# Performance work log

Hardware: AMD Instinct MI355X
Metric: run time of the kernel (lower is better)

## Reference

```python
import jax, jax.numpy as jnp
import numpy as np
import math

B, L = 32, 4096
INPUT_SIZE, QUERY_SIZE, VALUE_SIZE, H = 1024, 64, 256, 16
DV = INPUT_SIZE // H  # per-head value dim = 64


def setup_inputs() -> dict:
    key = jax.random.key(0)
    ks = jax.random.split(key, 7)
    s_q = 1.0 / math.sqrt(INPUT_SIZE)
    s_v = 1.0 / math.sqrt(VALUE_SIZE)
    return {
        "query": jax.random.normal(ks[0], (B, INPUT_SIZE), jnp.float32),
        "key": jax.random.normal(ks[1], (B, L, QUERY_SIZE), jnp.float32),
        "value": jax.random.normal(ks[2], (B, L, VALUE_SIZE), jnp.float32),
        # query_heads: Linear(input_size, head_num*query_size) with bias
        "Wq": jax.random.uniform(ks[3], (H * QUERY_SIZE, INPUT_SIZE), jnp.float32, -s_q, s_q),
        "bq": jax.random.uniform(ks[4], (H * QUERY_SIZE,), jnp.float32, -s_q, s_q),
        # value_proj: Linear(value_size, input_size) with bias (concatenate=True)
        "Wv": jax.random.uniform(ks[5], (INPUT_SIZE, VALUE_SIZE), jnp.float32, -s_v, s_v),
        "bv": jax.random.uniform(ks[6], (INPUT_SIZE,), jnp.float32, -s_v, s_v),
    }


def reference(query, key, value, Wq, bq, Wv, bv):
    # value projection: (B, L, input_size) -> (B, H, L, DV)
    v = jnp.einsum("bld,ed->ble", value, Wv) + bv
    v = v.reshape(B, L, H, DV).transpose(0, 2, 1, 3)
    # query projection: (B, input_size) -> (B, H, QUERY_SIZE)
    q = (query @ Wq.T + bq).reshape(B, H, QUERY_SIZE)
    # scores: (B, H, L); key shared across heads
    scores = jnp.einsum("bhd,bld->bhl", q, key) / math.sqrt(QUERY_SIZE)
    p = jax.nn.softmax(scores, axis=-1)
    # weighted sum: (B, H, DV) -> concat -> (B, input_size)
    out = jnp.einsum("bhl,bhld->bhd", p, v)
    return out.reshape(B, H * DV)
```

## Files before the change

### kernel.cpp

```cpp
#include <hip/hip_runtime.h>
#include <math.h>

#define B_   32
#define L_   4096
#define IN_  1024
#define QS_  64
#define VS_  256
#define H_   16

#define Q_OFF 0
#define M_OFF 32768

__device__ __forceinline__ float dot4(float4 a, float4 b) {
    return a.x*b.x + a.y*b.y + a.z*b.z + a.w*b.w;
}

__global__ __launch_bounds__(256) void qproj_kernel(
        const float* __restrict__ query, const float* __restrict__ Wq,
        const float* __restrict__ bq, float* __restrict__ ws) {
    const int t = threadIdx.x;
    const int g = blockIdx.x * 256 + t;
    const int o = g >> 2, sub = g & 3;
    const int b = o >> 10, c = o & 1023;

    const float4* wq4 = (const float4*)(Wq + (size_t)c * IN_) + sub * 64;
    const float4* q4  = (const float4*)(query + (size_t)b * IN_) + sub * 64;
    float4 acc = make_float4(0.f, 0.f, 0.f, 0.f);
    #pragma unroll 8
    for (int k = 0; k < 64; ++k) {
        float4 w = wq4[k], q = q4[k];
        acc.x += w.x * q.x; acc.y += w.y * q.y;
        acc.z += w.z * q.z; acc.w += w.w * q.w;
    }
    float r = acc.x + acc.y + acc.z + acc.w;
    r += __shfl_xor(r, 1);
    r += __shfl_xor(r, 2);
    if (sub == 0) ws[Q_OFF + b * 1024 + c] = (r + bq[c]) * 0.125f;
}

template<int CL>
__global__ __launch_bounds__(256, 4) void attn_chunk_kernel(
        const float* __restrict__ key, const float* __restrict__ value,
        float* __restrict__ ws) {
    constexpr int NCH = L_ / CL;
    constexpr int R   = CL / 64;
    constexpr int S_OFF   = M_OFF + B_ * NCH * H_;
    constexpr int CTX_OFF = S_OFF + B_ * NCH * H_;

    __shared__ float4 qs4[256];
    __shared__ float4 ps4[4 * CL];

    const int t  = threadIdx.x;
    const int ch = blockIdx.x, b = blockIdx.y;
    const int lm = t & 63, w = t >> 6;
    const int l0 = ch * CL;

    qs4[t] = ((const float4*)(ws + Q_OFF + (size_t)b * IN_))[t];
    __syncthreads();

    const float* keyb = key + ((size_t)b * L_ + l0) * QS_;
    float s[R][4];
    #pragma unroll
    for (int j = 0; j < R; ++j)
        #pragma unroll
        for (int hh = 0; hh < 4; ++hh) s[j][hh] = 0.f;

    #pragma unroll
    for (int e4 = 0; e4 < 16; ++e4) {
        float4 qv[4];
        #pragma unroll
        for (int hh = 0; hh < 4; ++hh) qv[hh] = qs4[(4 * w + hh) * 16 + e4];
        #pragma unroll
        for (int j = 0; j < R; ++j) {
            float4 kv = *(const float4*)(keyb + (size_t)(R * lm + j) * QS_ + e4 * 4);
            #pragma unroll
            for (int hh = 0; hh < 4; ++hh) s[j][hh] += dot4(kv, qv[hh]);
        }
    }

    float m[4];
    #pragma unroll
    for (int hh = 0; hh < 4; ++hh) {
        float v = s[0][hh];
        #pragma unroll
        for (int j = 1; j < R; ++j) v = fmaxf(v, s[j][hh]);
        #pragma unroll
        for (int off = 32; off >= 1; off >>= 1) v = fmaxf(v, __shfl_xor(v, off));
        m[hh] = v;
    }

    float p[R][4];
    #pragma unroll
    for (int j = 0; j < R; ++j)
        #pragma unroll
        for (int hh = 0; hh < 4; ++hh) p[j][hh] = __expf(s[j][hh] - m[hh]);

    float sum[4];
    #pragma unroll
    for (int hh = 0; hh < 4; ++hh) {
        float v = p[0][hh];
        #pragma unroll
        for (int j = 1; j < R; ++j) v += p[j][hh];
        #pragma unroll
        for (int off = 32; off >= 1; off >>= 1) v += __shfl_xor(v, off);
        sum[hh] = v;
    }
    if (lm == 0) {
        #pragma unroll
        for (int hh = 0; hh < 4; ++hh) {
            ws[M_OFF + (b * NCH + ch) * H_ + 4 * w + hh] = m[hh];
            ws[S_OFF + (b * NCH + ch) * H_ + 4 * w + hh] = sum[hh];
        }
    }

    #pragma unroll
    for (int j = 0; j < R; ++j)
        ps4[w * CL + R * lm + j] = make_float4(p[j][0], p[j][1], p[j][2], p[j][3]);

    float4 ctx[4];
    #pragma unroll
    for (int hh = 0; hh < 4; ++hh) ctx[hh] = make_float4(0.f, 0.f, 0.f, 0.f);

    const float*  valb = value + ((size_t)b * L_ + l0) * VS_;
    const float4* psw  = ps4 + w * CL;
    for (int i0 = 0; i0 < CL; i0 += 8) {
        float4 vv[8], pv[8];
        #pragma unroll
        for (int u = 0; u < 8; ++u)
            vv[u] = *(const float4*)(valb + (size_t)(i0 + u) * VS_ + 4 * lm);
        #pragma unroll
        for (int u = 0; u < 8; ++u) pv[u] = psw[i0 + u];
        #pragma unroll
        for (int u = 0; u < 8; ++u) {
            const float* ph = (const float*)&pv[u];
            #pragma unroll
            for (int hh = 0; hh < 4; ++hh) {
                ctx[hh].x += ph[hh] * vv[u].x;
                ctx[hh].y += ph[hh] * vv[u].y;
                ctx[hh].z += ph[hh] * vv[u].z;
                ctx[hh].w += ph[hh] * vv[u].w;
            }
        }
    }

    float* ctxw = ws + CTX_OFF + (size_t)((b * NCH + ch) * H_) * VS_;
    #pragma unroll
    for (int hh = 0; hh < 4; ++hh)
        *(float4*)(ctxw + (size_t)(4 * w + hh) * VS_ + 4 * lm) = ctx[hh];
}

template<int CL>
__global__ __launch_bounds__(256) void reduce_proj_kernel(
        const float* __restrict__ Wv, const float* __restrict__ bv,
        const float* __restrict__ ws, float* __restrict__ out) {
    constexpr int NCH = L_ / CL;
    constexpr int S_OFF   = M_OFF + B_ * NCH * H_;
    constexpr int CTX_OFF = S_OFF + B_ * NCH * H_;

    __shared__ __align__(16) float ctx_lds[VS_];
    const int t = threadIdx.x;
    const int b = blockIdx.x >> 4, h = blockIdx.x & 15;

    float M = -1e30f;
    #pragma unroll
    for (int c = 0; c < NCH; ++c)
        M = fmaxf(M, ws[M_OFF + (b * NCH + c) * H_ + h]);

    float S = 0.f, acc = 0.f;
    #pragma unroll 4
    for (int c = 0; c < NCH; ++c) {
        float wgt = __expf(ws[M_OFF + (b * NCH + c) * H_ + h] - M);
        S += ws[S_OFF + (b * NCH + c) * H_ + h] * wgt;
        acc += wgt * ws[CTX_OFF + ((size_t)(b * NCH + c) * H_ + h) * VS_ + t];
    }
    ctx_lds[t] = acc / S;
    __syncthreads();

    const int d = t >> 2, qq = t & 3;
    const float4* wv4 = (const float4*)(Wv + (size_t)(h * 64 + d) * VS_);
    const float4* cl4 = (const float4*)ctx_lds;
    float a = 0.f;
    #pragma unroll
    for (int i = 0; i < 16; ++i) a += dot4(wv4[qq * 16 + i], cl4[qq * 16 + i]);
    a += __shfl_xor(a, 1);
    a += __shfl_xor(a, 2);
    if (qq == 0) out[b * 1024 + h * 64 + d] = a + bv[h * 64 + d];
}

extern "C" void kernel_launch(void* const* d_in, const int* in_sizes, int n_in,
                              void* d_out, int out_size, void* d_ws, size_t ws_size,
                              hipStream_t stream) {
    (void)in_sizes; (void)n_in; (void)out_size;
    const float* query = (const float*)d_in[0];
    const float* key   = (const float*)d_in[1];
    const float* value = (const float*)d_in[2];
    const float* Wq    = (const float*)d_in[3];
    const float* bq    = (const float*)d_in[4];
    const float* Wv    = (const float*)d_in[5];
    const float* bv    = (const float*)d_in[6];
    float* out = (float*)d_out;
    float* ws  = (float*)d_ws;

    qproj_kernel<<<512, 256, 0, stream>>>(query, Wq, bq, ws);

    const size_t need128 = (size_t)(32768 + 2 * B_ * 32 * H_ + (size_t)B_ * 32 * H_ * VS_) * 4;
    if (ws_size >= need128) {
        attn_chunk_kernel<128><<<dim3(32, B_), 256, 0, stream>>>(key, value, ws);
        reduce_proj_kernel<128><<<B_ * H_, 256, 0, stream>>>(Wv, bv, ws, out);
    } else {
        attn_chunk_kernel<256><<<dim3(16, B_), 256, 0, stream>>>(key, value, ws);
        reduce_proj_kernel<256><<<B_ * H_, 256, 0, stream>>>(Wv, bv, ws, out);
    }
}
```

Before: 289.2 us.

## Widen attention blocks to 512 threads and split qproj dot products finer

The attention chunk kernel now uses 512 threads (8 waves), each wave handling 2 heads instead of 4. This halves per-thread score and context accumulators and doubles the waves available to hide value-load latency, at the cost of each wave re-reading the full value chunk (value traffic through cache doubles). The query projection splits each dot product across 16 lanes instead of 4 to spread work over 2048 blocks. The workspace-size fallback path for chunk 256 is removed, so the code assumes the workspace is large enough.

```diff
diff --git a/kernel.cpp b/kernel.cpp
--- a/kernel.cpp
+++ b/kernel.cpp
@@ -7,9 +7,13 @@
 #define QS_  64
 #define VS_  256
 #define H_   16
+#define CL_  128
+#define NCH_ 32
 
-#define Q_OFF 0
-#define M_OFF 32768
+#define Q_OFF   0
+#define M_OFF   32768
+#define S_OFF   (M_OFF + B_ * NCH_ * H_)
+#define CTX_OFF (S_OFF + B_ * NCH_ * H_)
 
 __device__ __forceinline__ float dot4(float4 a, float4 b) {
     return a.x*b.x + a.y*b.y + a.z*b.z + a.w*b.w;
@@ -20,14 +24,14 @@
         const float* __restrict__ bq, float* __restrict__ ws) {
     const int t = threadIdx.x;
     const int g = blockIdx.x * 256 + t;
-    const int o = g >> 2, sub = g & 3;
+    const int o = g >> 4, sub = g & 15;
     const int b = o >> 10, c = o & 1023;
 
-    const float4* wq4 = (const float4*)(Wq + (size_t)c * IN_) + sub * 64;
-    const float4* q4  = (const float4*)(query + (size_t)b * IN_) + sub * 64;
+    const float4* wq4 = (const float4*)(Wq + (size_t)c * IN_) + sub * 16;
+    const float4* q4  = (const float4*)(query + (size_t)b * IN_) + sub * 16;
     float4 acc = make_float4(0.f, 0.f, 0.f, 0.f);
-    #pragma unroll 8
-    for (int k = 0; k < 64; ++k) {
+    #pragma unroll
+    for (int k = 0; k < 16; ++k) {
         float4 w = wq4[k], q = q4[k];
         acc.x += w.x * q.x; acc.y += w.y * q.y;
         acc.z += w.z * q.z; acc.w += w.w * q.w;
@@ -35,143 +39,113 @@
     float r = acc.x + acc.y + acc.z + acc.w;
     r += __shfl_xor(r, 1);
     r += __shfl_xor(r, 2);
+    r += __shfl_xor(r, 4);
+    r += __shfl_xor(r, 8);
     if (sub == 0) ws[Q_OFF + b * 1024 + c] = (r + bq[c]) * 0.125f;
 }
 
-template<int CL>
-__global__ __launch_bounds__(256, 4) void attn_chunk_kernel(
+__global__ __launch_bounds__(512, 8) void attn_chunk_kernel(
         const float* __restrict__ key, const float* __restrict__ value,
         float* __restrict__ ws) {
-    constexpr int NCH = L_ / CL;
-    constexpr int R   = CL / 64;
-    constexpr int S_OFF   = M_OFF + B_ * NCH * H_;
-    constexpr int CTX_OFF = S_OFF + B_ * NCH * H_;
-
     __shared__ float4 qs4[256];
-    __shared__ float4 ps4[4 * CL];
+    __shared__ float2 ps2[8 * CL_];
 
     const int t  = threadIdx.x;
     const int ch = blockIdx.x, b = blockIdx.y;
     const int lm = t & 63, w = t >> 6;
-    const int l0 = ch * CL;
+    const int l0 = ch * CL_;
 
-    qs4[t] = ((const float4*)(ws + Q_OFF + (size_t)b * IN_))[t];
+    if (t < 256) qs4[t] = ((const float4*)(ws + Q_OFF + (size_t)b * IN_))[t];
     __syncthreads();
 
     const float* keyb = key + ((size_t)b * L_ + l0) * QS_;
-    float s[R][4];
-    #pragma unroll
-    for (int j = 0; j < R; ++j)
-        #pragma unroll
-        for (int hh = 0; hh < 4; ++hh) s[j][hh] = 0.f;
-
+    float s[2][2] = {{0.f, 0.f}, {0.f, 0.f}};
     #pragma unroll
     for (int e4 = 0; e4 < 16; ++e4) {
-        float4 qv[4];
+        float4 q0 = qs4[(2 * w) * 16 + e4];
+        float4 q1 = qs4[(2 * w + 1) * 16 + e4];
         #pragma unroll
-        for (int hh = 0; hh < 4; ++hh) qv[hh] = qs4[(4 * w + hh) * 16 + e4];
-        #pragma unroll
-        for (int j = 0; j < R; ++j) {
-            float4 kv = *(const float4*)(keyb + (size_t)(R * lm + j) * QS_ + e4 * 4);
-            #pragma unroll
-            for (int hh = 0; hh < 4; ++hh) s[j][hh] += dot4(kv, qv[hh]);
+        for (int j = 0; j < 2; ++j) {
+            float4 kv = *(const float4*)(keyb + (size_t)(2 * lm + j) * QS_ + e4 * 4);
+            s[j][0] += dot4(kv, q0);
+            s[j][1] += dot4(kv, q1);
         }
     }
 
-    float m[4];
+    float m[2], sum[2], p[2][2];
     #pragma unroll
-    for (int hh = 0; hh < 4; ++hh) {
-        float v = s[0][hh];
-        #pragma unroll
-        for (int j = 1; j < R; ++j) v = fmaxf(v, s[j][hh]);
+    for (int hh = 0; hh < 2; ++hh) {
+        float v = fmaxf(s[0][hh], s[1][hh]);
         #pragma unroll
         for (int off = 32; off >= 1; off >>= 1) v = fmaxf(v, __shfl_xor(v, off));
         m[hh] = v;
     }
-
-    float p[R][4];
     #pragma unroll
-    for (int j = 0; j < R; ++j)
+    for (int j = 0; j < 2; ++j)
         #pragma unroll
-        for (int hh = 0; hh < 4; ++hh) p[j][hh] = __expf(s[j][hh] - m[hh]);
-
-    float sum[4];
+        for (int hh = 0; hh < 2; ++hh) p[j][hh] = __expf(s[j][hh] - m[hh]);
     #pragma unroll
-    for (int hh = 0; hh < 4; ++hh) {
-        float v = p[0][hh];
-        #pragma unroll
-        for (int j = 1; j < R; ++j) v += p[j][hh];
+    for (int hh = 0; hh < 2; ++hh) {
+        float v = p[0][hh] + p[1][hh];
         #pragma unroll
         for (int off = 32; off >= 1; off >>= 1) v += __shfl_xor(v, off);
         sum[hh] = v;
     }
     if (lm == 0) {
         #pragma unroll
-        for (int hh = 0; hh < 4; ++hh) {
-            ws[M_OFF + (b * NCH + ch) * H_ + 4 * w + hh] = m[hh];
-            ws[S_OFF + (b * NCH + ch) * H_ + 4 * w + hh] = sum[hh];
+        for (int hh = 0; hh < 2; ++hh) {
+            ws[M_OFF + (b * NCH_ + ch) * H_ + 2 * w + hh] = m[hh];
+            ws[S_OFF + (b * NCH_ + ch) * H_ + 2 * w + hh] = sum[hh];
         }
     }
 
     #pragma unroll
-    for (int j = 0; j < R; ++j)
-        ps4[w * CL + R * lm + j] = make_float4(p[j][0], p[j][1], p[j][2], p[j][3]);
+    for (int j = 0; j < 2; ++j)
+        ps2[w * CL_ + 2 * lm + j] = make_float2(p[j][0], p[j][1]);
 
-    float4 ctx[4];
-    #pragma unroll
-    for (int hh = 0; hh < 4; ++hh) ctx[hh] = make_float4(0.f, 0.f, 0.f, 0.f);
-
+    float4 ctx0 = make_float4(0.f, 0.f, 0.f, 0.f);
+    float4 ctx1 = make_float4(0.f, 0.f, 0.f, 0.f);
     const float*  valb = value + ((size_t)b * L_ + l0) * VS_;
-    const float4* psw  = ps4 + w * CL;
-    for (int i0 = 0; i0 < CL; i0 += 8) {
-        float4 vv[8], pv[8];
+    const float2* psw  = ps2 + w * CL_;
+    for (int i0 = 0; i0 < CL_; i0 += 4) {
+        float4 vv[4]; float2 pv[4];
         #pragma unroll
-        for (int u = 0; u < 8; ++u)
+        for (int u = 0; u < 4; ++u)
             vv[u] = *(const float4*)(valb + (size_t)(i0 + u) * VS_ + 4 * lm);
         #pragma unroll
-        for (int u = 0; u < 8; ++u) pv[u] = psw[i0 + u];
+        for (int u = 0; u < 4; ++u) pv[u] = psw[i0 + u];
         #pragma unroll
-        for (int u = 0; u < 8; ++u) {
-            const float* ph = (const float*)&pv[u];
-            #pragma unroll
-            for (int hh = 0; hh < 4; ++hh) {
-                ctx[hh].x += ph[hh] * vv[u].x;
-                ctx[hh].y += ph[hh] * vv[u].y;
-                ctx[hh].z += ph[hh] * vv[u].z;
-                ctx[hh].w += ph[hh] * vv[u].w;
-            }
+        for (int u = 0; u < 4; ++u) {
+            ctx0.x += pv[u].x * vv[u].x; ctx0.y += pv[u].x * vv[u].y;
+            ctx0.z += pv[u].x * vv[u].z; ctx0.w += pv[u].x * vv[u].w;
+            ctx1.x += pv[u].y * vv[u].x; ctx1.y += pv[u].y * vv[u].y;
+            ctx1.z += pv[u].y * vv[u].z; ctx1.w += pv[u].y * vv[u].w;
         }
     }
 
-    float* ctxw = ws + CTX_OFF + (size_t)((b * NCH + ch) * H_) * VS_;
-    #pragma unroll
-    for (int hh = 0; hh < 4; ++hh)
-        *(float4*)(ctxw + (size_t)(4 * w + hh) * VS_ + 4 * lm) = ctx[hh];
+    float* ctxw = ws + CTX_OFF + (size_t)((b * NCH_ + ch) * H_) * VS_;
+    *(float4*)(ctxw + (size_t)(2 * w) * VS_ + 4 * lm)     = ctx0;
+    *(float4*)(ctxw + (size_t)(2 * w + 1) * VS_ + 4 * lm) = ctx1;
 }
 
-template<int CL>
 __global__ __launch_bounds__(256) void reduce_proj_kernel(
         const float* __restrict__ Wv, const float* __restrict__ bv,
         const float* __restrict__ ws, float* __restrict__ out) {
-    constexpr int NCH = L_ / CL;
-    constexpr int S_OFF   = M_OFF + B_ * NCH * H_;
-    constexpr int CTX_OFF = S_OFF + B_ * NCH * H_;
-
     __shared__ __align__(16) float ctx_lds[VS_];
     const int t = threadIdx.x;
     const int b = blockIdx.x >> 4, h = blockIdx.x & 15;
 
     float M = -1e30f;
     #pragma unroll
-    for (int c = 0; c < NCH; ++c)
-        M = fmaxf(M, ws[M_OFF + (b * NCH + c) * H_ + h]);
+    for (int c = 0; c < NCH_; ++c)
+        M = fmaxf(M, ws[M_OFF + (b * NCH_ + c) * H_ + h]);
 
     float S = 0.f, acc = 0.f;
     #pragma unroll 4
-    for (int c = 0; c < NCH; ++c) {
-        float wgt = __expf(ws[M_OFF + (b * NCH + c) * H_ + h] - M);
-        S += ws[S_OFF + (b * NCH + c) * H_ + h] * wgt;
-        acc += wgt * ws[CTX_OFF + ((size_t)(b * NCH + c) * H_ + h) * VS_ + t];
+    for (int c = 0; c < NCH_; ++c) {
+        float wgt = __expf(ws[M_OFF + (b * NCH_ + c) * H_ + h] - M);
+        S += ws[S_OFF + (b * NCH_ + c) * H_ + h] * wgt;
+        acc += wgt * ws[CTX_OFF + ((size_t)(b * NCH_ + c) * H_ + h) * VS_ + t];
     }
     ctx_lds[t] = acc / S;
     __syncthreads();
@@ -190,7 +164,7 @@
 extern "C" void kernel_launch(void* const* d_in, const int* in_sizes, int n_in,
                               void* d_out, int out_size, void* d_ws, size_t ws_size,
                               hipStream_t stream) {
-    (void)in_sizes; (void)n_in; (void)out_size;
+    (void)in_sizes; (void)n_in; (void)out_size; (void)ws_size;
     const float* query = (const float*)d_in[0];
     const float* key   = (const float*)d_in[1];
     const float* value = (const float*)d_in[2];
@@ -201,14 +175,7 @@
     float* out = (float*)d_out;
     float* ws  = (float*)d_ws;
 
-    qproj_kernel<<<512, 256, 0, stream>>>(query, Wq, bq, ws);
-
-    const size_t need128 = (size_t)(32768 + 2 * B_ * 32 * H_ + (size_t)B_ * 32 * H_ * VS_) * 4;
-    if (ws_size >= need128) {
-        attn_chunk_kernel<128><<<dim3(32, B_), 256, 0, stream>>>(key, value, ws);
-        reduce_proj_kernel<128><<<B_ * H_, 256, 0, stream>>>(Wv, bv, ws, out);
-    } else {
-        attn_chunk_kernel<256><<<dim3(16, B_), 256, 0, stream>>>(key, value, ws);
-        reduce_proj_kernel<256><<<B_ * H_, 256, 0, stream>>>(Wv, bv, ws, out);
-    }
+    qproj_kernel<<<2048, 256, 0, stream>>>(query, Wq, bq, ws);
+    attn_chunk_kernel<<<dim3(NCH_, B_), 512, 0, stream>>>(key, value, ws);
+    reduce_proj_kernel<<<B_ * H_, 256, 0, stream>>>(Wv, bv, ws, out);
 }
```

Result: slower. 370.6 us (+28.1%).
